# Kernel optimization log

Measured on AMD Instinct MI355X. Metric: run time of the kernel, lower is better.

## Reference

```python
import jax, jax.numpy as jnp
import numpy as np
from jax import lax

K = 16  # number of KNN neighbors (fixed in module)


def _knn_neighbors(x, k):
    # x: (B, 3, N) point coordinates -> neighbor coords (B, 3, N, K)
    inner = jnp.einsum('bdn,bdm->bnm', x, x)          # (B, N, N)
    sq = jnp.sum(x * x, axis=1)                        # (B, N)
    d2 = sq[:, :, None] + sq[:, None, :] - 2.0 * inner  # pairwise sq dists (B, N, N)
    _, nbr_idx = lax.top_k(-d2, k)                     # k nearest (incl. self), (B, N, K)
    # gather neighbor coordinates: expand x to (B, 3, 1, N), idx to (B, 1, N, K)
    neighbor = jnp.take_along_axis(x[:, :, None, :], nbr_idx[:, None, :, :], axis=3)
    return neighbor  # (B, 3, N, K)


def _down_index(neighbor, x, npts_ds):
    # center-diff saliency: sum of squared offsets to K neighbors per point
    diff = neighbor - x[:, :, :, None]                 # (B, 3, N, K)
    score = jnp.sum(diff * diff, axis=(1, 3))          # (B, N)
    _, idx = lax.top_k(score, npts_ds)                 # (B, npts_ds)
    return idx


def setup_inputs() -> dict:
    key = jax.random.key(0)
    k1, k2 = jax.random.split(key)
    B, N, C = 8, 4096, 128
    x = jax.random.normal(k1, (B, 3, N), dtype=jnp.float32)
    y = jax.random.normal(k2, (B, C, N), dtype=jnp.float32)
    return {"x": x, "y": y, "npts_ds": 2048}


def reference(x, y, npts_ds):
    B, _, N = x.shape
    C = y.shape[1]
    neighbor = _knn_neighbors(x, K)                    # ops.group(x, K, 'neighbor')
    idx = _down_index(neighbor, x, npts_ds)            # ops.down_index(...), (B, npts_ds)
    idx3 = jnp.broadcast_to(idx[:, None, :], (B, 3, npts_ds))
    idxC = jnp.broadcast_to(idx[:, None, :], (B, C, npts_ds))
    top_k_xyz = jnp.take_along_axis(x, idx3, axis=2)    # (B, 3, npts_ds)
    top_k_points = jnp.take_along_axis(y, idxC, axis=2)  # (B, C, npts_ds)
    return (top_k_xyz, top_k_points)
```

## Files before the change

kernel.cpp:

```cpp
#include <hip/hip_runtime.h>
#include <math.h>

#define BATCH 8
#define NPTS 4096
#define CHAN 128
#define KNN 16
#define SPLIT 4
#define CHUNK (NPTS / SPLIT)
#define ISPLIT 4
#define QCH (CHUNK / ISPLIT)
#define PTILE 128
#define EPC 24
#define RSPLIT 4
#define RCHUNK (NPTS / RSPLIT)

typedef unsigned long long u64;

__device__ __forceinline__ u64 pack_key(float d2, int idx) {
  unsigned b = __float_as_uint(d2);
  b ^= (unsigned)((int)b >> 31) | 0x80000000u;
  return ((u64)b << 32) | (unsigned)idx;
}

__device__ __forceinline__ float d2_ref(float4 q, float ppx, float ppy,
                                        float ppz, float psq) {
  float inner = __fadd_rn(__fadd_rn(__fmul_rn(ppx, q.x), __fmul_rn(ppy, q.y)),
                          __fmul_rn(ppz, q.z));
  return __fsub_rn(__fadd_rn(psq, q.w), __fmul_rn(2.0f, inner));
}

__device__ __forceinline__ void ce_asc(u64& x, u64& y) {
  bool sw = y < x;
  u64 lo = sw ? y : x;
  u64 hi = sw ? x : y;
  x = lo;
  y = hi;
}

__device__ __forceinline__ void batcher_sort16_u64(u64 a[16]) {
#define CE(i, j) ce_asc(a[i], a[j])
  CE(0, 8); CE(1, 9); CE(2, 10); CE(3, 11);
  CE(4, 12); CE(5, 13); CE(6, 14); CE(7, 15);
  CE(0, 4); CE(1, 5); CE(2, 6); CE(3, 7);
  CE(8, 12); CE(9, 13); CE(10, 14); CE(11, 15);
  CE(4, 8); CE(5, 9); CE(6, 10); CE(7, 11);
  CE(0, 2); CE(1, 3); CE(4, 6); CE(5, 7);
  CE(8, 10); CE(9, 11); CE(12, 14); CE(13, 15);
  CE(2, 8); CE(3, 9); CE(6, 12); CE(7, 13);
  CE(2, 4); CE(3, 5); CE(6, 8); CE(7, 9); CE(10, 12); CE(11, 13);
  CE(0, 1); CE(2, 3); CE(4, 5); CE(6, 7);
  CE(8, 9); CE(10, 11); CE(12, 13); CE(14, 15);
  CE(1, 8); CE(3, 10); CE(5, 12); CE(7, 14);
  CE(1, 4); CE(3, 6); CE(5, 8); CE(7, 10); CE(9, 12); CE(11, 14);
  CE(1, 2); CE(3, 4); CE(5, 6); CE(7, 8); CE(9, 10); CE(11, 12); CE(13, 14);
#undef CE
}

__device__ __forceinline__ void bitonic_sort32(u64 a[32]) {
#pragma unroll
  for (int k = 2; k <= 32; k <<= 1) {
#pragma unroll
    for (int j = k >> 1; j > 0; j >>= 1) {
#pragma unroll
      for (int i = 0; i < 32; ++i) {
        int l = i ^ j;
        if (l > i) {
          if ((i & k) == 0) ce_asc(a[i], a[l]);
          else              ce_asc(a[l], a[i]);
        }
      }
    }
  }
}

__device__ __forceinline__ void merge_keep16(u64 T[16], const u64 A[16]) {
  u64 nt[16];
#pragma unroll
  for (int i = 0; i < 16; ++i) {
    u64 a = A[15 - i];
    nt[i] = (a < T[i]) ? a : T[i];
  }
#pragma unroll
  for (int j = 8; j > 0; j >>= 1) {
#pragma unroll
    for (int i = 0; i < 16; ++i) {
      int l = i ^ j;
      if (l > i) ce_asc(nt[i], nt[l]);
    }
  }
#pragma unroll
  for (int i = 0; i < 16; ++i) T[i] = nt[i];
}

__device__ __forceinline__ void ce_i32(int& x, int& y) {
  int lo = (x < y) ? x : y;
  int hi = (x < y) ? y : x;
  x = lo;
  y = hi;
}

__device__ __forceinline__ void batcher_sort16_i32(int a[16]) {
#define CE(i, j) ce_i32(a[i], a[j])
  CE(0, 8); CE(1, 9); CE(2, 10); CE(3, 11);
  CE(4, 12); CE(5, 13); CE(6, 14); CE(7, 15);
  CE(0, 4); CE(1, 5); CE(2, 6); CE(3, 7);
  CE(8, 12); CE(9, 13); CE(10, 14); CE(11, 15);
  CE(4, 8); CE(5, 9); CE(6, 10); CE(7, 11);
  CE(0, 2); CE(1, 3); CE(4, 6); CE(5, 7);
  CE(8, 10); CE(9, 11); CE(12, 14); CE(13, 15);
  CE(2, 8); CE(3, 9); CE(6, 12); CE(7, 13);
  CE(2, 4); CE(3, 5); CE(6, 8); CE(7, 9); CE(10, 12); CE(11, 13);
  CE(0, 1); CE(2, 3); CE(4, 5); CE(6, 7);
  CE(8, 9); CE(10, 11); CE(12, 13); CE(14, 15);
  CE(1, 8); CE(3, 10); CE(5, 12); CE(7, 14);
  CE(1, 4); CE(3, 6); CE(5, 8); CE(7, 10); CE(9, 12); CE(11, 14);
  CE(1, 2); CE(3, 4); CE(5, 6); CE(7, 8); CE(9, 10); CE(11, 12); CE(13, 14);
#undef CE
}

__device__ __forceinline__ void merge_keep16_i32(int T[16], const int A[16]) {
  int nt[16];
#pragma unroll
  for (int i = 0; i < 16; ++i) {
    int a = A[15 - i];
    nt[i] = (a < T[i]) ? a : T[i];
  }
#pragma unroll
  for (int j = 8; j > 0; j >>= 1) {
#pragma unroll
    for (int i = 0; i < 16; ++i) {
      int l = i ^ j;
      if (l > i) ce_i32(nt[i], nt[l]);
    }
  }
#pragma unroll
  for (int i = 0; i < 16; ++i) T[i] = nt[i];
}

__global__ __launch_bounds__(512) void knn_partial_kernel(
    const float* __restrict__ x, u64* __restrict__ pkey) {
  const int s = blockIdx.x % SPLIT;
  const int ntile = (blockIdx.x / SPLIT) % (NPTS / PTILE);
  const int b = blockIdx.x / (SPLIT * (NPTS / PTILE));
  const int p = threadIdx.x & (PTILE - 1);
  const int q4 = threadIdx.x >> 7;
  __shared__ float4 xs[CHUNK];
  __shared__ u64 ubuf[2048];

  const float* xb = x + (size_t)b * 3 * NPTS;
  for (int i = threadIdx.x; i < CHUNK; i += 512) {
    int gm = s * CHUNK + i;
    float px = xb[gm];
    float py = xb[NPTS + gm];
    float pz = xb[2 * NPTS + gm];
    float sq = __fadd_rn(__fadd_rn(__fmul_rn(px, px), __fmul_rn(py, py)),
                         __fmul_rn(pz, pz));
    xs[i] = make_float4(px, py, pz, sq);
  }

  const int n = ntile * PTILE + p;
  float ppx = xb[n];
  float ppy = xb[NPTS + n];
  float ppz = xb[2 * NPTS + n];
  float psq = __fadd_rn(__fadd_rn(__fmul_rn(ppx, ppx), __fmul_rn(ppy, ppy)),
                        __fmul_rn(ppz, ppz));
  __syncthreads();

  const int cbase = q4 * QCH;

  int T[16];
#pragma unroll
  for (int i = 0; i < 16; ++i) T[i] = 0x7FFFFFFF;
  int r17 = 0x7FFFFFFF;

#pragma unroll 1
  for (int base = 0; base < QCH; base += 16) {
    int A[16];
#pragma unroll
    for (int t = 0; t < 16; ++t) {
      float4 q = xs[cbase + base + t];
      int bits = __float_as_int(d2_ref(q, ppx, ppy, ppz, psq));
      A[t] = (bits & 0xFFFFFF00) | (base + t);
    }
    batcher_sort16_i32(A);
    int u[16];
#pragma unroll
    for (int i = 0; i < 16; ++i) {
      int a = A[15 - i];
      u[i] = (T[i] < a) ? a : T[i];
    }
#pragma unroll
    for (int w = 8; w > 0; w >>= 1) {
#pragma unroll
      for (int i = 0; i < 16; ++i) {
        if (i < w) u[i] = (u[i] < u[i + w]) ? u[i] : u[i + w];
      }
    }
    r17 = (r17 < u[0]) ? r17 : u[0];
    merge_keep16_i32(T, A);
  }

  const int tau = T[15] & 0xFFFFFF00;
  const bool slow = ((r17 & 0xFFFFFF00) == tau);

  u64 K[16];
  if (!slow) {
#pragma unroll
    for (int j = 0; j < 16; ++j) {
      int loc = cbase + (T[j] & 255);
      float4 q = xs[loc];
      float d2 = d2_ref(q, ppx, ppy, ppz, psq);
      K[j] = pack_key(d2, s * CHUNK + loc);
    }
    batcher_sort16_u64(K);
  } else {
    unsigned char* myb =
        reinterpret_cast<unsigned char*>(ubuf) + (unsigned)threadIdx.x * EPC;
    int cnt = 0;
#pragma unroll 4
    for (int m = 0; m < QCH; ++m) {
      float4 q = xs[cbase + m];
      int tb = __float_as_int(d2_ref(q, ppx, ppy, ppz, psq)) & 0xFFFFFF00;
      if (tb <= tau) {
        myb[cnt < EPC - 1 ? cnt : EPC - 1] = (unsigned char)m;
        ++cnt;
      }
    }
    u64 KK[32];
#pragma unroll
    for (int j = 0; j < EPC; ++j) {
      int loc = cbase + myb[j];
      float4 q = xs[loc];
      float d2 = d2_ref(q, ppx, ppy, ppz, psq);
      u64 k = pack_key(d2, s * CHUNK + loc);
      KK[j] = (j < cnt) ? k : ~0ull;
    }
#pragma unroll
    for (int j = EPC; j < 32; ++j) KK[j] = ~0ull;
    bitonic_sort32(KK);
#pragma unroll
    for (int j = 0; j < 16; ++j) K[j] = KK[j];
  }

  __syncthreads();
  u64(*L)[PTILE] = reinterpret_cast<u64(*)[PTILE]>(ubuf);
#pragma unroll 1
  for (int r = 1; r <= 3; ++r) {
    if (q4 == r) {
#pragma unroll
      for (int j = 0; j < 16; ++j) L[j][p] = K[j];
    }
    __syncthreads();
    if (q4 == 0) {
      u64 A64[16];
#pragma unroll
      for (int j = 0; j < 16; ++j) A64[j] = L[j][p];
      merge_keep16(K, A64);
    }
    __syncthreads();
  }
  if (q4 == 0) {
    u64* pb = pkey + ((size_t)(b * SPLIT + s) * KNN) * NPTS + n;
#pragma unroll
    for (int j = 0; j < 16; ++j) pb[(size_t)j * NPTS] = K[j];
  }
}

__global__ __launch_bounds__(256) void merge_score_kernel(
    const float* __restrict__ x, const u64* __restrict__ pkey,
    float* __restrict__ score, int* __restrict__ cnt) {
  const int tile = blockIdx.x % (NPTS / 64);
  const int b = blockIdx.x / (NPTS / 64);
  const int g = threadIdx.x >> 2;
  const int s = threadIdx.x & 3;
  const int n = tile * 64 + g;

  if (threadIdx.x < 64)
    cnt[(size_t)b * NPTS + tile * 64 + threadIdx.x] = 0;

  u64 T[16];
  {
    const u64* pb = pkey + ((size_t)(b * SPLIT + s) * KNN) * NPTS + n;
#pragma unroll
    for (int j = 0; j < 16; ++j) T[j] = pb[(size_t)j * NPTS];
  }

  u64 A[16];
#pragma unroll
  for (int j = 0; j < 16; ++j)
    A[j] = (u64)__shfl_xor((long long)T[j], 1);
  merge_keep16(T, A);
#pragma unroll
  for (int j = 0; j < 16; ++j)
    A[j] = (u64)__shfl_xor((long long)T[j], 2);
  merge_keep16(T, A);

  const float* xb = x + (size_t)b * 3 * NPTS;
  float P = 0.0f;
  if (s < 3) {
    const float* xd = xb + (size_t)s * NPTS;
    const float pc = xd[n];
    float r[8];
#pragma unroll
    for (int j = 0; j < 8; ++j) {
      float c0 = xd[(int)(unsigned)T[j]];
      float c1 = xd[(int)(unsigned)T[j + 8]];
      float e0 = __fsub_rn(c0, pc);
      float e1 = __fsub_rn(c1, pc);
      r[j] = __fadd_rn(__fmul_rn(e0, e0), __fmul_rn(e1, e1));
    }
    float t0 = __fadd_rn(r[0], r[1]);
    float t1 = __fadd_rn(r[2], r[3]);
    float t2 = __fadd_rn(r[4], r[5]);
    float t3 = __fadd_rn(r[6], r[7]);
    P = __fadd_rn(__fadd_rn(t0, t1), __fadd_rn(t2, t3));
  }
  float Pa = __shfl_xor(P, 1);
  float Pb = __shfl_xor(P, 2);
  if (s == 0)
    score[(size_t)b * NPTS + n] = __fadd_rn(__fadd_rn(P, Pa), Pb);
}

__global__ __launch_bounds__(256) void rank_partial_kernel(
    const float* __restrict__ score, int* __restrict__ cnt) {
  const int s = blockIdx.x % RSPLIT;
  const int ntile = (blockIdx.x / RSPLIT) % (NPTS / 256);
  const int b = blockIdx.x / (RSPLIT * (NPTS / 256));
  __shared__ float4 sv[RCHUNK / 4];

  const float* sb = score + (size_t)b * NPTS;
  const float4* sb4 = reinterpret_cast<const float4*>(sb + s * RCHUNK);
  for (int i = threadIdx.x; i < RCHUNK / 4; i += 256) sv[i] = sb4[i];

  const int n = ntile * 256 + threadIdx.x;
  const float sn = sb[n];
  __syncthreads();

  int c = 0;
#pragma unroll 4
  for (int v = 0; v < RCHUNK / 4; ++v) {
    float4 f = sv[v];
    int gm = s * RCHUNK + 4 * v;
    c += (f.x > sn) || (f.x == sn && gm < n);
    c += (f.y > sn) || (f.y == sn && gm + 1 < n);
    c += (f.z > sn) || (f.z == sn && gm + 2 < n);
    c += (f.w > sn) || (f.w == sn && gm + 3 < n);
  }
  atomicAdd(&cnt[(size_t)b * NPTS + n], c);
}

__global__ __launch_bounds__(256) void rank_scatter_kernel(
    const int* __restrict__ cnt, int* __restrict__ sel, int npts) {
  int t = blockIdx.x * 256 + threadIdx.x;
  int b = t / NPTS;
  int n = t % NPTS;
  int c = cnt[t];
  if (c < npts) sel[(size_t)b * npts + c] = n;
}

__global__ __launch_bounds__(256) void gather_kernel(
    const float* __restrict__ x, const float* __restrict__ y,
    const int* __restrict__ sel, float* __restrict__ out, int npts,
    int total0, int total) {
  int tid = blockIdx.x * blockDim.x + threadIdx.x;
  if (tid >= total) return;
  if (tid < total0) {
    int j = tid % npts;
    int rest = tid / npts;
    int d = rest % 3;
    int b = rest / 3;
    int src = sel[b * npts + j];
    out[tid] = x[((size_t)b * 3 + d) * NPTS + src];
  } else {
    int t = tid - total0;
    int j = t % npts;
    int rest = t / npts;
    int c = rest % CHAN;
    int b = rest / CHAN;
    int src = sel[b * npts + j];
    out[tid] = y[((size_t)b * CHAN + c) * NPTS + src];
  }
}

extern "C" void kernel_launch(void* const* d_in, const int* in_sizes, int n_in,
                              void* d_out, int out_size, void* d_ws,
                              size_t ws_size, hipStream_t stream) {
  const float* x = (const float*)d_in[0];
  const float* y = (const float*)d_in[1];
  float* out = (float*)d_out;

  const int npts = out_size / (BATCH * (3 + CHAN));

  char* w = (char*)d_ws;
  u64* pkey = (u64*)w;
  w += sizeof(u64) * (size_t)BATCH * SPLIT * KNN * NPTS;
  float* score = (float*)w;
  w += sizeof(float) * (size_t)BATCH * NPTS;
  int* cnt = (int*)w;
  w += sizeof(int) * (size_t)BATCH * NPTS;
  int* sel = (int*)w;

  knn_partial_kernel<<<BATCH * (NPTS / PTILE) * SPLIT, 512, 0, stream>>>(
      x, pkey);
  merge_score_kernel<<<BATCH * (NPTS / 64), 256, 0, stream>>>(x, pkey, score,
                                                              cnt);
  rank_partial_kernel<<<BATCH * (NPTS / 256) * RSPLIT, 256, 0, stream>>>(
      score, cnt);
  rank_scatter_kernel<<<BATCH * NPTS / 256, 256, 0, stream>>>(cnt, sel, npts);

  const int total0 = BATCH * 3 * npts;
  gather_kernel<<<(out_size + 255) / 256, 256, 0, stream>>>(
      x, y, sel, out, npts, total0, out_size);
}
```

Measured before the change: 246.9 us.

## Fuse rank count and scatter into one kernel; halve KNN point tile

Merges the split rank-count kernel and the scatter kernel into one. Each block loads a whole batch's scores into shared memory, two half-blocks count over halves, and they combine through shared memory instead of global atomics. This removes the count buffer, its zero-init in the merge kernel, one launch and the atomicAdd traffic, but every block now reloads the full score array. Separately, the KNN partial kernel tile shrinks from 128 to 64 points with 256-thread blocks, doubling the block count and halving shared scratch, which may change occupancy.

```diff
diff --git a/kernel.cpp b/kernel.cpp
--- a/kernel.cpp
+++ b/kernel.cpp
@@ -9,10 +9,8 @@
 #define CHUNK (NPTS / SPLIT)
 #define ISPLIT 4
 #define QCH (CHUNK / ISPLIT)
-#define PTILE 128
+#define PTILE 64
 #define EPC 24
-#define RSPLIT 4
-#define RCHUNK (NPTS / RSPLIT)
 
 typedef unsigned long long u64;
 
@@ -137,18 +135,18 @@
   for (int i = 0; i < 16; ++i) T[i] = nt[i];
 }
 
-__global__ __launch_bounds__(512) void knn_partial_kernel(
+__global__ __launch_bounds__(256) void knn_partial_kernel(
     const float* __restrict__ x, u64* __restrict__ pkey) {
   const int s = blockIdx.x % SPLIT;
   const int ntile = (blockIdx.x / SPLIT) % (NPTS / PTILE);
   const int b = blockIdx.x / (SPLIT * (NPTS / PTILE));
   const int p = threadIdx.x & (PTILE - 1);
-  const int q4 = threadIdx.x >> 7;
+  const int q4 = threadIdx.x >> 6;
   __shared__ float4 xs[CHUNK];
-  __shared__ u64 ubuf[2048];
+  __shared__ u64 ubuf[1024];
 
   const float* xb = x + (size_t)b * 3 * NPTS;
-  for (int i = threadIdx.x; i < CHUNK; i += 512) {
+  for (int i = threadIdx.x; i < CHUNK; i += 256) {
     int gm = s * CHUNK + i;
     float px = xb[gm];
     float py = xb[NPTS + gm];
@@ -268,15 +266,12 @@
 
 __global__ __launch_bounds__(256) void merge_score_kernel(
     const float* __restrict__ x, const u64* __restrict__ pkey,
-    float* __restrict__ score, int* __restrict__ cnt) {
+    float* __restrict__ score) {
   const int tile = blockIdx.x % (NPTS / 64);
   const int b = blockIdx.x / (NPTS / 64);
   const int g = threadIdx.x >> 2;
   const int s = threadIdx.x & 3;
   const int n = tile * 64 + g;
-
-  if (threadIdx.x < 64)
-    cnt[(size_t)b * NPTS + tile * 64 + threadIdx.x] = 0;
 
   u64 T[16];
   {
@@ -321,41 +316,40 @@
     score[(size_t)b * NPTS + n] = __fadd_rn(__fadd_rn(P, Pa), Pb);
 }
 
-__global__ __launch_bounds__(256) void rank_partial_kernel(
-    const float* __restrict__ score, int* __restrict__ cnt) {
-  const int s = blockIdx.x % RSPLIT;
-  const int ntile = (blockIdx.x / RSPLIT) % (NPTS / 256);
-  const int b = blockIdx.x / (RSPLIT * (NPTS / 256));
-  __shared__ float4 sv[RCHUNK / 4];
+__global__ __launch_bounds__(256) void rank_scatter_kernel(
+    const float* __restrict__ score, int* __restrict__ sel, int npts) {
+  const int tile = blockIdx.x % (NPTS / 128);
+  const int b = blockIdx.x / (NPTS / 128);
+  const int p = threadIdx.x & 127;
+  const int h = threadIdx.x >> 7;
+  __shared__ float4 sv[NPTS / 4];
+  __shared__ int cpart[128];
 
   const float* sb = score + (size_t)b * NPTS;
-  const float4* sb4 = reinterpret_cast<const float4*>(sb + s * RCHUNK);
-  for (int i = threadIdx.x; i < RCHUNK / 4; i += 256) sv[i] = sb4[i];
-
-  const int n = ntile * 256 + threadIdx.x;
+  const float4* sb4 = reinterpret_cast<const float4*>(sb);
+  for (int i = threadIdx.x; i < NPTS / 4; i += 256) sv[i] = sb4[i];
+
+  const int n = tile * 128 + p;
   const float sn = sb[n];
   __syncthreads();
 
   int c = 0;
+  const int v0 = h * (NPTS / 8);
 #pragma unroll 4
-  for (int v = 0; v < RCHUNK / 4; ++v) {
+  for (int v = v0; v < v0 + NPTS / 8; ++v) {
     float4 f = sv[v];
-    int gm = s * RCHUNK + 4 * v;
+    int gm = 4 * v;
     c += (f.x > sn) || (f.x == sn && gm < n);
     c += (f.y > sn) || (f.y == sn && gm + 1 < n);
     c += (f.z > sn) || (f.z == sn && gm + 2 < n);
     c += (f.w > sn) || (f.w == sn && gm + 3 < n);
   }
-  atomicAdd(&cnt[(size_t)b * NPTS + n], c);
-}
-
-__global__ __launch_bounds__(256) void rank_scatter_kernel(
-    const int* __restrict__ cnt, int* __restrict__ sel, int npts) {
-  int t = blockIdx.x * 256 + threadIdx.x;
-  int b = t / NPTS;
-  int n = t % NPTS;
-  int c = cnt[t];
-  if (c < npts) sel[(size_t)b * npts + c] = n;
+  if (h == 1) cpart[p] = c;
+  __syncthreads();
+  if (h == 0) {
+    c += cpart[p];
+    if (c < npts) sel[(size_t)b * npts + c] = n;
+  }
 }
 
 __global__ __launch_bounds__(256) void gather_kernel(
@@ -396,18 +390,13 @@
   w += sizeof(u64) * (size_t)BATCH * SPLIT * KNN * NPTS;
   float* score = (float*)w;
   w += sizeof(float) * (size_t)BATCH * NPTS;
-  int* cnt = (int*)w;
-  w += sizeof(int) * (size_t)BATCH * NPTS;
   int* sel = (int*)w;
 
-  knn_partial_kernel<<<BATCH * (NPTS / PTILE) * SPLIT, 512, 0, stream>>>(
+  knn_partial_kernel<<<BATCH * (NPTS / PTILE) * SPLIT, 256, 0, stream>>>(
       x, pkey);
-  merge_score_kernel<<<BATCH * (NPTS / 64), 256, 0, stream>>>(x, pkey, score,
-                                                              cnt);
-  rank_partial_kernel<<<BATCH * (NPTS / 256) * RSPLIT, 256, 0, stream>>>(
-      score, cnt);
-  rank_scatter_kernel<<<BATCH * NPTS / 256, 256, 0, stream>>>(cnt, sel, npts);
-
+  merge_score_kernel<<<BATCH * (NPTS / 64), 256, 0, stream>>>(x, pkey, score);
+  rank_scatter_kernel<<<BATCH * (NPTS / 128), 256, 0, stream>>>(score, sel,
+                                                                npts);
   const int total0 = BATCH * 3 * npts;
   gather_kernel<<<(out_size + 255) / 256, 256, 0, stream>>>(
       x, y, sel, out, npts, total0, out_size);
```

Measured after the change: 257.6 us. 1.04x slower.
